# Optimization experiments

Hardware: AMD Instinct MI355X
Metric: run time of the kernel (lower is better)

The kernel has to match this reference:

```python
import jax, jax.numpy as jnp
import numpy as np

EPS = 1e-5

def setup_inputs() -> dict:
    key = jax.random.key(0)
    ks = jax.random.split(key, 12)
    b, C, Hx = 8, 1024, 28          # x: (b, C, Hx, Hx); y: (b, C//2, 2*Hx, 2*Hx)
    C2 = C // 2
    r = C2 // 7                      # fc bottleneck = 73
    f32 = jnp.float32
    inp = {
        'y': jax.random.normal(ks[0], (b, C2, 2*Hx, 2*Hx), f32),
        'x': jax.random.normal(ks[1], (b, C, Hx, Hx), f32),
        'fc1_w': jax.random.normal(ks[2], (r, C2), f32) * 0.02,
        'fc2_w': jax.random.normal(ks[3], (C2, r), f32) * 0.02,
        'conv_w': jax.random.normal(ks[4], (C2, C, 1, 1), f32) * 0.02,
        'conv_b': jnp.zeros((C2,), f32),
        'conv1_w': jax.random.normal(ks[5], (C2, C2 * 4, 1, 1), f32) * 0.02,
        'conv1_b': jnp.zeros((C2,), f32),
        'bn_gamma': jnp.ones((C2,), f32),
        'bn_beta': jnp.zeros((C2,), f32),
        'bn_mean': jnp.zeros((C2,), f32),
        'bn_var': jnp.ones((C2,), f32),
        'dw_w': jax.random.normal(ks[6], (C, 1, 3, 3), f32) * 0.1,  # depthwise, groups=C
        'dw_b': jnp.zeros((C,), f32),
    }
    return inp

def reference(y, x, fc1_w, fc2_w, conv_w, conv_b, conv1_w, conv1_b,
              bn_gamma, bn_beta, bn_mean, bn_var, dw_w, dw_b):
    def bn(t):  # BatchNorm2d in eval mode (running stats); same bn module reused twice
        return (t - bn_mean[:, None, None]) * jax.lax.rsqrt(bn_var[:, None, None] + EPS) \
               * bn_gamma[:, None, None] + bn_beta[:, None, None]
    # SE channel attention on y
    s = jnp.mean(y, axis=(2, 3))                              # (b, C2) GAP
    s = jax.nn.relu(s @ fc1_w.T) @ fc2_w.T                    # bias-free FCs
    y1 = y * jax.nn.sigmoid(s)[:, :, None, None]
    # depthwise 3x3 conv on x
    x1 = jax.lax.conv_general_dilated(
        x, dw_w, (1, 1), ((1, 1), (1, 1)),
        feature_group_count=x.shape[1],
        dimension_numbers=('NCHW', 'OIHW', 'NCHW')) + dw_b[None, :, None, None]
    # np.cov per (b, c) map: rows are variables, ddof=1 -> (Xc @ Xc^T)/(W-1)
    Wn = x1.shape[-1]
    xc = x1 - jnp.mean(x1, axis=-1, keepdims=True)
    x2 = jnp.einsum('bchw,bcgw->bchg', xc, xc) / (Wn - 1)     # (b, C, H, H)
    # 1x1 conv C->C2, bn, sigmoid
    x2 = jnp.einsum('bchw,oc->bohw', x2, conv_w[:, :, 0, 0]) + conv_b[None, :, None, None]
    x2 = jax.nn.sigmoid(bn(x2))
    # bilinear upsample x2 (half-pixel == torch align_corners=False)
    def up2(t):
        bb, cc, hh, ww = t.shape
        return jax.image.resize(t, (bb, cc, 2 * hh, 2 * ww), method='bilinear')
    x_up = up2(x)
    x2_up = up2(x2)
    cat = jnp.concatenate([y1, x2_up, x_up], axis=1)          # (b, 4*C2, 2H, 2W)
    out = jnp.einsum('bchw,oc->bohw', cat, conv1_w[:, :, 0, 0]) + conv1_b[None, :, None, None]
    return jax.nn.relu(bn(out))
```

## Files before the change

### kernel.cpp

```cpp
#include <hip/hip_runtime.h>
#include <math.h>

#define EPSV 1e-5f
#define B 8
#define C 1024
#define C2 512
#define RK 73
#define HW 784
#define QW 3136

typedef __attribute__((ext_vector_type(8))) short bf16x8;
typedef __attribute__((ext_vector_type(4))) float f32x4;

__device__ __forceinline__ unsigned short f2bf(float f) {
    unsigned u = __float_as_uint(f);
    return (unsigned short)((u + 0x7fffu + ((u >> 16) & 1u)) >> 16);
}
__device__ __forceinline__ float ld_f(const float* p) { return *p; }
__device__ __forceinline__ float ld_f(const unsigned short* p) {
    return __uint_as_float(((unsigned)*p) << 16);
}
__device__ __forceinline__ void ld4f(const float* p, float* d) {
    float4 v = *(const float4*)p;
    d[0] = v.x; d[1] = v.y; d[2] = v.z; d[3] = v.w;
}
__device__ __forceinline__ void ld4f(const unsigned short* p, float* d) {
    uint2 u = *(const uint2*)p;
    d[0] = __uint_as_float((u.x & 0xffffu) << 16);
    d[1] = __uint_as_float(u.x & 0xffff0000u);
    d[2] = __uint_as_float((u.y & 0xffffu) << 16);
    d[3] = __uint_as_float(u.y & 0xffff0000u);
}

__global__ void zero_s0(float* __restrict__ s0) {
    s0[blockIdx.x * 256 + threadIdx.x] = 0.f;
}

__global__ void se_fc_kernel(const float* __restrict__ s0,
                             const float* __restrict__ fc1_w,
                             const float* __restrict__ fc2_w,
                             float* __restrict__ att) {
    int b = blockIdx.x;
    __shared__ float sv[C2];
    __shared__ float hv[RK];
    for (int i = threadIdx.x; i < C2; i += 256) sv[i] = s0[b * C2 + i] * (1.0f / QW);
    __syncthreads();
    if (threadIdx.x < RK) {
        float acc = 0.f;
        const float4* wr4 = (const float4*)(fc1_w + threadIdx.x * C2);
        const float4* sv4 = (const float4*)sv;
#pragma unroll 16
        for (int k = 0; k < C2 / 4; ++k) {
            float4 w4 = wr4[k], s4 = sv4[k];
            acc += w4.x * s4.x + w4.y * s4.y + w4.z * s4.z + w4.w * s4.w;
        }
        hv[threadIdx.x] = fmaxf(acc, 0.f);
    }
    __syncthreads();
    for (int o = threadIdx.x; o < C2; o += 256) {
        float acc = 0.f;
        const float* wr = fc2_w + o * RK;
#pragma unroll
        for (int j = 0; j < RK; ++j) acc += wr[j] * hv[j];
        att[b * C2 + o] = 1.f / (1.f + expf(-acc));
    }
}

__global__ void dwcov_kernel(const float* __restrict__ x,
                             const float* __restrict__ dw_w,
                             const float* __restrict__ dw_b,
                             unsigned short* __restrict__ cov) {
    int bc = blockIdx.x;
    int c = bc & (C - 1);
    __shared__ float xs[HW];
    __shared__ __align__(16) float x1[HW];
    __shared__ float rm[28];
    const float* px = x + (size_t)bc * HW;
    for (int i = threadIdx.x; i < HW; i += 256) xs[i] = px[i];
    float wk[9];
#pragma unroll
    for (int j = 0; j < 9; ++j) wk[j] = dw_w[c * 9 + j];
    float bias = dw_b[c];
    __syncthreads();
    for (int p = threadIdx.x; p < HW; p += 256) {
        int h = p / 28, w = p - h * 28;
        float acc = bias;
#pragma unroll
        for (int dh = 0; dh < 3; ++dh) {
            int hh = h + dh - 1;
            if (hh < 0 || hh >= 28) continue;
#pragma unroll
            for (int dw = 0; dw < 3; ++dw) {
                int ww = w + dw - 1;
                if (ww < 0 || ww >= 28) continue;
                acc += xs[hh * 28 + ww] * wk[dh * 3 + dw];
            }
        }
        x1[p] = acc;
    }
    __syncthreads();
    if (threadIdx.x < 28) {
        float s = 0.f;
        for (int w = 0; w < 28; ++w) s += x1[threadIdx.x * 28 + w];
        rm[threadIdx.x] = s * (1.f / 28.f);
    }
    __syncthreads();
    unsigned short* pc = cov + (size_t)bc * HW;
    for (int p = threadIdx.x; p < HW; p += 256) {
        int h = p / 28, g = p - h * 28;
        float mh = rm[h], mg = rm[g];
        const float4* xh = (const float4*)&x1[h * 28];
        const float4* xg = (const float4*)&x1[g * 28];
        float acc = 0.f;
#pragma unroll
        for (int w4 = 0; w4 < 7; ++w4) {
            float4 a = xh[w4], bq = xg[w4];
            acc += (a.x - mh) * (bq.x - mg);
            acc += (a.y - mh) * (bq.y - mg);
            acc += (a.z - mh) * (bq.z - mg);
            acc += (a.w - mh) * (bq.w - mg);
        }
        pc[p] = f2bf(acc * (1.f / 27.f));
    }
}

__global__ void pack_w(const float* __restrict__ conv_w, const float* __restrict__ conv_b,
                       const float* __restrict__ conv1_w, const float* __restrict__ conv1_b,
                       const float* __restrict__ bn_g, const float* __restrict__ bn_b,
                       const float* __restrict__ bn_m, const float* __restrict__ bn_v,
                       const float* __restrict__ att,
                       unsigned short* __restrict__ w0b, unsigned short* __restrict__ w1y,
                       unsigned short* __restrict__ w1pT,
                       float* __restrict__ sA, float* __restrict__ sB0, float* __restrict__ sB1) {
    int o = blockIdx.x, t = threadIdx.x;
    {
        int c4 = t * 4;
        float4 w4 = *(const float4*)&conv_w[(size_t)o * C + c4];
        unsigned short pk[4] = { f2bf(w4.x), f2bf(w4.y), f2bf(w4.z), f2bf(w4.w) };
        *(uint2*)&w0b[(size_t)o * C + c4] = *(uint2*)pk;
    }
#pragma unroll
    for (int i = 0; i < 2; ++i) {
        int e = t + i * 256;
        if (e < 384) {
            int c4 = e * 4;
            float4 w4 = *(const float4*)&conv1_w[(size_t)o * 2048 + 512 + c4];
            unsigned short pk[4] = { f2bf(w4.x), f2bf(w4.y), f2bf(w4.z), f2bf(w4.w) };
            *(uint2*)&w1pT[(size_t)o * 1536 + c4] = *(uint2*)pk;
        }
    }
#pragma unroll
    for (int i = 0; i < 4; ++i) {
        int e = t + i * 256;
        int bb = e >> 7, c4 = (e & 127) * 4;
        float4 w4 = *(const float4*)&conv1_w[(size_t)o * 2048 + c4];
        float4 a4 = *(const float4*)&att[bb * C2 + c4];
        unsigned short pk[4] = { f2bf(w4.x * a4.x), f2bf(w4.y * a4.y),
                                 f2bf(w4.z * a4.z), f2bf(w4.w * a4.w) };
        *(uint2*)&w1y[((size_t)bb * C2 + o) * C2 + c4] = *(uint2*)pk;
    }
    if (t == 0) {
        float sc = rsqrtf(bn_v[o] + EPSV) * bn_g[o];
        float bi = bn_b[o] - bn_m[o] * sc;
        sA[o] = sc;
        sB0[o] = conv_b[o] * sc + bi;
        sB1[o] = conv1_b[o] * sc + bi;
    }
}

template<typename ST, bool GAP>
__global__ __launch_bounds__(256)
void transpose_pass(const ST* __restrict__ src, unsigned short* __restrict__ dst,
                    float* __restrict__ s0,
                    int rows, int cols, int dpitch, int doff) {
    int b = blockIdx.z;
    int c0 = blockIdx.y * 64, p0 = blockIdx.x * 64;
    __shared__ float ts[64][65];
    int tid = threadIdx.x;
    int pl4 = (tid & 15) * 4, rr = tid >> 4;
    const ST* sb = src + ((size_t)b * rows + c0) * cols + p0;
    if (p0 + pl4 < cols) {
#pragma unroll
        for (int j = 0; j < 4; ++j) {
            int cl = rr + j * 16;
            float d[4];
            ld4f(&sb[(size_t)cl * cols + pl4], d);
            ts[cl][pl4 + 0] = d[0]; ts[cl][pl4 + 1] = d[1];
            ts[cl][pl4 + 2] = d[2]; ts[cl][pl4 + 3] = d[3];
        }
    }
    __syncthreads();
    int pl2b = tid >> 3, cl0 = (tid & 7) * 8;
#pragma unroll
    for (int j = 0; j < 2; ++j) {
        int pl2 = pl2b + j * 32;
        if (p0 + pl2 < cols) {
            unsigned short pk[8];
#pragma unroll
            for (int i = 0; i < 8; ++i) pk[i] = f2bf(ts[cl0 + i][pl2]);
            *(uint4*)&dst[((size_t)b * cols + p0 + pl2) * dpitch + doff + c0 + cl0] = *(uint4*)pk;
        }
    }
    if (GAP) {
        if (tid < 64) {
            float s = 0.f;
#pragma unroll
            for (int i = 0; i < 64; ++i) s += ts[tid][i];
            atomicAdd(&s0[b * rows + c0 + tid], s);
        }
    }
}

template<int MODE, int K>
__global__ __launch_bounds__(256)
void mfma_gemm(const unsigned short* __restrict__ wpk,
               const unsigned short* __restrict__ bsrc,
               const unsigned short* __restrict__ Pb,
               const float* __restrict__ sA, const float* __restrict__ sB,
               void* __restrict__ outv) {
    constexpr int NIT = K / 32;
    constexpr int NT  = (MODE == 2) ? 49 : 98;
    constexpr int QN = NT >> 3, REM = NT & 7;
    int bx = blockIdx.x;
    int r = bx & 7, ii = bx >> 3;
    int og = ii & 7, s = ii >> 3;
    int cnt = QN + (r < REM ? 1 : 0);
    if (s >= cnt) return;
    int t = (r < REM ? r * (QN + 1) : REM * (QN + 1) + (r - REM) * QN) + s;
    int o0 = og * 64;
    int n0 = t * 64;
    int b = blockIdx.z;
    union SM {
        struct { __align__(16) unsigned short Wt[2][2048]; __align__(16) unsigned short At[2][2048]; } s;
        float pt[(MODE == 2) ? 64 * 84 : 4];
    };
    __shared__ SM sm;
    int tid = threadIdx.x;
    int lane = tid & 63, wv = tid >> 6;
    int ln = lane & 15, quad = lane >> 4;
    int o_w = (wv >> 1) * 32, q_w = (wv & 1) * 32;
    int swr = tid >> 2, swk = (tid & 3) * 8;
    int stw = swr * 32 + (((tid & 3) ^ ((swr >> 1) & 3)) << 3);
    int rq  = (quad ^ ((ln >> 1) & 3)) << 3;
    const unsigned short* wp = (MODE == 2) ? wpk + (size_t)b * C2 * C2 : wpk;
    const unsigned short* wg = wp + (size_t)(o0 + swr) * K + swk;
    const unsigned short* bg = bsrc + ((size_t)((MODE == 2) ? b * QW : 0) + n0 + swr) * K + swk;

    uint4 stA_a, stA_b, stB_a, stB_b, stC_a, stC_b, stD_a, stD_b;

#define LD_STAGE(P, CH) {                                                   \
        P##_a = *(const uint4*)(wg + (size_t)(CH) * 32);                    \
        P##_b = *(const uint4*)(bg + (size_t)(CH) * 32); }

#define ST_STAGE(P, BUF) {                                                  \
        *(uint4*)&sm.s.Wt[BUF][stw] = P##_a;                                \
        *(uint4*)&sm.s.At[BUF][stw] = P##_b; }

#define GEMM_BODY(BUF, P, CHW, CHL) {                                               \
        bf16x8 af0 = *(const bf16x8*)&sm.s.Wt[BUF][(o_w + ln) * 32 + rq];           \
        bf16x8 af1 = *(const bf16x8*)&sm.s.Wt[BUF][(o_w + 16 + ln) * 32 + rq];      \
        bf16x8 bf0 = *(const bf16x8*)&sm.s.At[BUF][(q_w + ln) * 32 + rq];           \
        bf16x8 bf1 = *(const bf16x8*)&sm.s.At[BUF][(q_w + 16 + ln) * 32 + rq];      \
        acc[0][0] = __builtin_amdgcn_mfma_f32_16x16x32_bf16(af0, bf0, acc[0][0], 0, 0, 0); \
        acc[0][1] = __builtin_amdgcn_mfma_f32_16x16x32_bf16(af0, bf1, acc[0][1], 0, 0, 0); \
        acc[1][0] = __builtin_amdgcn_mfma_f32_16x16x32_bf16(af1, bf0, acc[1][0], 0, 0, 0); \
        acc[1][1] = __builtin_amdgcn_mfma_f32_16x16x32_bf16(af1, bf1, acc[1][1], 0, 0, 0); \
        if ((CHW) < NIT) {                                                          \
            ST_STAGE(P, (BUF) ^ 1)                                                  \
            if ((CHL) < NIT) LD_STAGE(P, (CHL))                                     \
            asm volatile("s_waitcnt lgkmcnt(0)" ::: "memory");                      \
            __builtin_amdgcn_s_barrier();                                           \
            __builtin_amdgcn_sched_barrier(0);                                      \
        } }

    LD_STAGE(stA, 0)
    ST_STAGE(stA, 0)
    LD_STAGE(stB, 1)
    LD_STAGE(stC, 2)
    LD_STAGE(stD, 3)
    LD_STAGE(stA, 4)
    asm volatile("s_waitcnt lgkmcnt(0)" ::: "memory");
    __builtin_amdgcn_s_barrier();
    __builtin_amdgcn_sched_barrier(0);

    f32x4 acc[2][2] = {};
    for (int i2 = 0; i2 < NIT; i2 += 4) {
        GEMM_BODY(0, stB, i2 + 1, i2 + 5)
        GEMM_BODY(1, stC, i2 + 2, i2 + 6)
        GEMM_BODY(0, stD, i2 + 3, i2 + 7)
        GEMM_BODY(1, stA, i2 + 4, i2 + 8)
    }
#undef GEMM_BODY
#undef ST_STAGE
#undef LD_STAGE

    if (MODE == 2) {
        float* outp = (float*)outv;
        int h0 = n0 / 56;
        int hmin = (h0 & 1) ? (h0 >> 1) : max(0, (h0 >> 1) - 1);
        float stv[21];
#pragma unroll
        for (int j = 0; j < 21; ++j) {
            int e = tid + j * 256;
            int o_l = e / 84, rem = e - o_l * 84;
            int s2 = rem / 28, w = rem - s2 * 28;
            int row = min(hmin + s2, 27);
            stv[j] = ld_f(&Pb[((size_t)b * C2 + o0 + o_l) * HW + row * 28 + w]);
        }
        __syncthreads();
#pragma unroll
        for (int j = 0; j < 21; ++j) sm.pt[tid + j * 256] = stv[j];
        __syncthreads();
#pragma unroll
        for (int nt = 0; nt < 2; ++nt) {
            int q = n0 + q_w + nt * 16 + ln;
            int hq = q / 56, wq = q - hq * 56;
            int hm = hq >> 1, wm = wq >> 1;
            int hn = (hq & 1) ? min(hm + 1, 27) : max(hm - 1, 0);
            int wn_ = (wq & 1) ? min(wm + 1, 27) : max(wm - 1, 0);
            int rm_ = (hm - hmin) * 28, rn_ = (hn - hmin) * 28;
#pragma unroll
            for (int mt = 0; mt < 2; ++mt)
#pragma unroll
                for (int reg = 0; reg < 4; ++reg) {
                    int ol = o_w + mt * 16 + quad * 4 + reg;
                    int o = o0 + ol;
                    const float* Pt = &sm.pt[ol * 84];
                    float up = 0.5625f * Pt[rm_ + wm] + 0.1875f * (Pt[rm_ + wn_] + Pt[rn_ + wm])
                             + 0.0625f * Pt[rn_ + wn_];
                    float v = (acc[mt][nt][reg] + up) * sA[o] + sB[o];
                    outp[((size_t)b * C2 + o) * QW + q] = fmaxf(v, 0.f);
                }
        }
    } else if (MODE == 0) {
        unsigned short* outp = (unsigned short*)outv;
#pragma unroll
        for (int nt = 0; nt < 2; ++nt) {
            int n = n0 + q_w + nt * 16 + ln;
#pragma unroll
            for (int mt = 0; mt < 2; ++mt) {
                int ob = o0 + o_w + mt * 16 + quad * 4;
                unsigned short pk[4];
#pragma unroll
                for (int reg = 0; reg < 4; ++reg) {
                    int o = ob + reg;
                    float v = acc[mt][nt][reg] * sA[o] + sB[o];
                    pk[reg] = f2bf(1.f / (1.f + expf(-v)));
                }
                *(uint2*)&outp[(size_t)n * 1536 + ob] = *(uint2*)pk;
            }
        }
    } else {
        unsigned short* outp = (unsigned short*)outv;
#pragma unroll
        for (int nt = 0; nt < 2; ++nt) {
            int n = n0 + q_w + nt * 16 + ln;
            int be = n / HW, pe = n - be * HW;
#pragma unroll
            for (int mt = 0; mt < 2; ++mt)
#pragma unroll
                for (int reg = 0; reg < 4; ++reg) {
                    int o = o0 + o_w + mt * 16 + quad * 4 + reg;
                    outp[((size_t)be * C2 + o) * HW + pe] = f2bf(acc[mt][nt][reg]);
                }
        }
    }
}

extern "C" void kernel_launch(void* const* d_in, const int* in_sizes, int n_in,
                              void* d_out, int out_size, void* d_ws, size_t ws_size,
                              hipStream_t stream) {
    const float* y       = (const float*)d_in[0];
    const float* x       = (const float*)d_in[1];
    const float* fc1_w   = (const float*)d_in[2];
    const float* fc2_w   = (const float*)d_in[3];
    const float* conv_w  = (const float*)d_in[4];
    const float* conv_b  = (const float*)d_in[5];
    const float* conv1_w = (const float*)d_in[6];
    const float* conv1_b = (const float*)d_in[7];
    const float* bn_g    = (const float*)d_in[8];
    const float* bn_b    = (const float*)d_in[9];
    const float* bn_m    = (const float*)d_in[10];
    const float* bn_v    = (const float*)d_in[11];
    const float* dw_w    = (const float*)d_in[12];
    const float* dw_b    = (const float*)d_in[13];
    float* out = (float*)d_out;

    unsigned short* cov_bf = (unsigned short*)d_out;
    unsigned short* covT   = cov_bf + (size_t)B * C * HW;
    unsigned short* BcatT  = covT + (size_t)B * HW * C;

    float* ws  = (float*)d_ws;
    float* s0  = ws;
    float* att = ws + 4096;
    float* sA  = ws + 8192;
    float* sB0 = ws + 8704;
    float* sB1 = ws + 9216;
    unsigned short* w0b  = (unsigned short*)(ws + 9728);
    unsigned short* w1y  = w0b + (size_t)C2 * C;
    unsigned short* w1pT = w1y + (size_t)B * C2 * C2;
    unsigned short* yT   = w1pT + (size_t)C2 * 1536;
    unsigned short* Pb   = yT + (size_t)B * QW * C2;

    zero_s0<<<16, 256, 0, stream>>>(s0);
    transpose_pass<float, true><<<dim3(49, 8, B), 256, 0, stream>>>(
        y, yT, s0, C2, QW, C2, 0);
    se_fc_kernel<<<B, 256, 0, stream>>>(s0, fc1_w, fc2_w, att);
    pack_w<<<C2, 256, 0, stream>>>(conv_w, conv_b, conv1_w, conv1_b,
                                   bn_g, bn_b, bn_m, bn_v, att,
                                   w0b, w1y, w1pT, sA, sB0, sB1);
    dwcov_kernel<<<B * C, 256, 0, stream>>>(x, dw_w, dw_b, cov_bf);
    transpose_pass<float, false><<<dim3(13, 16, B), 256, 0, stream>>>(
        x, BcatT, nullptr, C, HW, 1536, 512);
    transpose_pass<unsigned short, false><<<dim3(13, 16, B), 256, 0, stream>>>(
        cov_bf, covT, nullptr, C, HW, C, 0);
    mfma_gemm<0, 1024><<<dim3(832), 256, 0, stream>>>(w0b, covT, nullptr, sA, sB0, BcatT);
    mfma_gemm<1, 1536><<<dim3(832), 256, 0, stream>>>(w1pT, BcatT, nullptr, sA, sB0, Pb);
    mfma_gemm<2, 512><<<dim3(448, 1, B), 256, 0, stream>>>(w1y, yT, Pb, sA, sB1, out);
}
```

Baseline: 294.4 us.

## Double GEMM K-step to 64 and exploit covariance symmetry

The MFMA GEMM now stages 64-wide K chunks per pipeline step instead of 32. Each step issues eight MFMAs per barrier, with a new XOR swizzle over 8 segments and doubled LDS buffers. This halves the number of barrier and stage iterations but raises register and LDS use, which may reduce occupancy. Separately, the covariance kernel computes only the lower triangle (406 entries) and writes each value to both symmetric positions, cutting its dot-product work roughly in half at the cost of a sqrt-based index decode.

```diff
diff --git a/kernel.cpp b/kernel.cpp
--- a/kernel.cpp
+++ b/kernel.cpp
@@ -106,8 +106,11 @@
     }
     __syncthreads();
     unsigned short* pc = cov + (size_t)bc * HW;
-    for (int p = threadIdx.x; p < HW; p += 256) {
-        int h = p / 28, g = p - h * 28;
+    for (int idx = threadIdx.x; idx < 406; idx += 256) {
+        int h = (int)((sqrtf((float)(8 * idx + 1)) - 1.f) * 0.5f);
+        while ((h + 1) * (h + 2) / 2 <= idx) ++h;
+        while (h * (h + 1) / 2 > idx) --h;
+        int g = idx - h * (h + 1) / 2;
         float mh = rm[h], mg = rm[g];
         const float4* xh = (const float4*)&x1[h * 28];
         const float4* xg = (const float4*)&x1[g * 28];
@@ -120,7 +123,9 @@
             acc += (a.z - mh) * (bq.z - mg);
             acc += (a.w - mh) * (bq.w - mg);
         }
-        pc[p] = f2bf(acc * (1.f / 27.f));
+        unsigned short v = f2bf(acc * (1.f / 27.f));
+        pc[h * 28 + g] = v;
+        pc[g * 28 + h] = v;
     }
 }
 
@@ -218,7 +223,7 @@
                const unsigned short* __restrict__ Pb,
                const float* __restrict__ sA, const float* __restrict__ sB,
                void* __restrict__ outv) {
-    constexpr int NIT = K / 32;
+    constexpr int NIT = K / 64;
     constexpr int NT  = (MODE == 2) ? 49 : 98;
     constexpr int QN = NT >> 3, REM = NT & 7;
     int bx = blockIdx.x;
@@ -231,7 +236,7 @@
     int n0 = t * 64;
     int b = blockIdx.z;
     union SM {
-        struct { __align__(16) unsigned short Wt[2][2048]; __align__(16) unsigned short At[2][2048]; } s;
+        struct { __align__(16) unsigned short Wt[2][4096]; __align__(16) unsigned short At[2][4096]; } s;
         float pt[(MODE == 2) ? 64 * 84 : 4];
     };
     __shared__ SM sm;
@@ -239,32 +244,49 @@
     int lane = tid & 63, wv = tid >> 6;
     int ln = lane & 15, quad = lane >> 4;
     int o_w = (wv >> 1) * 32, q_w = (wv & 1) * 32;
-    int swr = tid >> 2, swk = (tid & 3) * 8;
-    int stw = swr * 32 + (((tid & 3) ^ ((swr >> 1) & 3)) << 3);
-    int rq  = (quad ^ ((ln >> 1) & 3)) << 3;
+    int r_ = tid >> 2, cq = tid & 3;
+    int stw0 = r_ * 64 + ((( cq << 1)      ^ (r_ & 7)) << 3);
+    int stw1 = r_ * 64 + ((((cq << 1) | 1) ^ (r_ & 7)) << 3);
+    int rq0 = (( quad      ^ (ln & 7)) << 3);
+    int rq1 = (((4 | quad) ^ (ln & 7)) << 3);
     const unsigned short* wp = (MODE == 2) ? wpk + (size_t)b * C2 * C2 : wpk;
-    const unsigned short* wg = wp + (size_t)(o0 + swr) * K + swk;
-    const unsigned short* bg = bsrc + ((size_t)((MODE == 2) ? b * QW : 0) + n0 + swr) * K + swk;
-
-    uint4 stA_a, stA_b, stB_a, stB_b, stC_a, stC_b, stD_a, stD_b;
+    const unsigned short* wg = wp + (size_t)(o0 + r_) * K + cq * 16;
+    const unsigned short* bg = bsrc + ((size_t)((MODE == 2) ? b * QW : 0) + n0 + r_) * K + cq * 16;
+
+    uint4 stA_a0, stA_a1, stA_b0, stA_b1;
+    uint4 stB_a0, stB_a1, stB_b0, stB_b1;
+    uint4 stC_a0, stC_a1, stC_b0, stC_b1;
+    uint4 stD_a0, stD_a1, stD_b0, stD_b1;
 
 #define LD_STAGE(P, CH) {                                                   \
-        P##_a = *(const uint4*)(wg + (size_t)(CH) * 32);                    \
-        P##_b = *(const uint4*)(bg + (size_t)(CH) * 32); }
+        P##_a0 = *(const uint4*)(wg + (size_t)(CH) * 64);                   \
+        P##_a1 = *(const uint4*)(wg + (size_t)(CH) * 64 + 8);               \
+        P##_b0 = *(const uint4*)(bg + (size_t)(CH) * 64);                   \
+        P##_b1 = *(const uint4*)(bg + (size_t)(CH) * 64 + 8); }
 
 #define ST_STAGE(P, BUF) {                                                  \
-        *(uint4*)&sm.s.Wt[BUF][stw] = P##_a;                                \
-        *(uint4*)&sm.s.At[BUF][stw] = P##_b; }
+        *(uint4*)&sm.s.Wt[BUF][stw0] = P##_a0;                              \
+        *(uint4*)&sm.s.Wt[BUF][stw1] = P##_a1;                              \
+        *(uint4*)&sm.s.At[BUF][stw0] = P##_b0;                              \
+        *(uint4*)&sm.s.At[BUF][stw1] = P##_b1; }
 
 #define GEMM_BODY(BUF, P, CHW, CHL) {                                               \
-        bf16x8 af0 = *(const bf16x8*)&sm.s.Wt[BUF][(o_w + ln) * 32 + rq];           \
-        bf16x8 af1 = *(const bf16x8*)&sm.s.Wt[BUF][(o_w + 16 + ln) * 32 + rq];      \
-        bf16x8 bf0 = *(const bf16x8*)&sm.s.At[BUF][(q_w + ln) * 32 + rq];           \
-        bf16x8 bf1 = *(const bf16x8*)&sm.s.At[BUF][(q_w + 16 + ln) * 32 + rq];      \
-        acc[0][0] = __builtin_amdgcn_mfma_f32_16x16x32_bf16(af0, bf0, acc[0][0], 0, 0, 0); \
-        acc[0][1] = __builtin_amdgcn_mfma_f32_16x16x32_bf16(af0, bf1, acc[0][1], 0, 0, 0); \
-        acc[1][0] = __builtin_amdgcn_mfma_f32_16x16x32_bf16(af1, bf0, acc[1][0], 0, 0, 0); \
-        acc[1][1] = __builtin_amdgcn_mfma_f32_16x16x32_bf16(af1, bf1, acc[1][1], 0, 0, 0); \
+        bf16x8 a0 = *(const bf16x8*)&sm.s.Wt[BUF][(o_w + ln) * 64 + rq0];           \
+        bf16x8 a1 = *(const bf16x8*)&sm.s.Wt[BUF][(o_w + 16 + ln) * 64 + rq0];      \
+        bf16x8 b0 = *(const bf16x8*)&sm.s.At[BUF][(q_w + ln) * 64 + rq0];           \
+        bf16x8 b1 = *(const bf16x8*)&sm.s.At[BUF][(q_w + 16 + ln) * 64 + rq0];      \
+        bf16x8 a2 = *(const bf16x8*)&sm.s.Wt[BUF][(o_w + ln) * 64 + rq1];           \
+        bf16x8 a3 = *(const bf16x8*)&sm.s.Wt[BUF][(o_w + 16 + ln) * 64 + rq1];      \
+        bf16x8 b2 = *(const bf16x8*)&sm.s.At[BUF][(q_w + ln) * 64 + rq1];           \
+        bf16x8 b3 = *(const bf16x8*)&sm.s.At[BUF][(q_w + 16 + ln) * 64 + rq1];      \
+        acc[0][0] = __builtin_amdgcn_mfma_f32_16x16x32_bf16(a0, b0, acc[0][0], 0, 0, 0); \
+        acc[0][1] = __builtin_amdgcn_mfma_f32_16x16x32_bf16(a0, b1, acc[0][1], 0, 0, 0); \
+        acc[1][0] = __builtin_amdgcn_mfma_f32_16x16x32_bf16(a1, b0, acc[1][0], 0, 0, 0); \
+        acc[1][1] = __builtin_amdgcn_mfma_f32_16x16x32_bf16(a1, b1, acc[1][1], 0, 0, 0); \
+        acc[0][0] = __builtin_amdgcn_mfma_f32_16x16x32_bf16(a2, b2, acc[0][0], 0, 0, 0); \
+        acc[0][1] = __builtin_amdgcn_mfma_f32_16x16x32_bf16(a2, b3, acc[0][1], 0, 0, 0); \
+        acc[1][0] = __builtin_amdgcn_mfma_f32_16x16x32_bf16(a3, b2, acc[1][0], 0, 0, 0); \
+        acc[1][1] = __builtin_amdgcn_mfma_f32_16x16x32_bf16(a3, b3, acc[1][1], 0, 0, 0); \
         if ((CHW) < NIT) {                                                          \
             ST_STAGE(P, (BUF) ^ 1)                                                  \
             if ((CHL) < NIT) LD_STAGE(P, (CHL))                                     \
```

New measurement: 284.8 us. -3.3%, faster.
